# Optimization experiments

Hardware: AMD Instinct MI355X
Metric: run time of the kernel (lower is better)

The kernel has to match this reference:

```python
import jax, jax.numpy as jnp
import numpy as np

B = 32; NPG = 500; N = B * NPG; E = 256000; F = 1024; OD = 128
DD = 80; TD = 32; NH = 4; DH = TD // NH; DFF = 128; NL = 2
LSUB = 128; MAXLEN = 4 * LSUB
NEG = -1e9; SLOPE = 0.01; EPS = 1e-5


def setup_inputs() -> dict:
    key = jax.random.key(0)
    ks = iter(jax.random.split(key, 64))
    nrm = lambda *s: jax.random.normal(next(ks), s, jnp.float32)
    w = lambda *s: nrm(*s) * 0.02
    inp = {}
    inp["pro1_x"] = nrm(N, F)
    inp["pro2_x"] = nrm(N, F)
    inp["pro1_edge_index"] = jax.random.randint(next(ks), (2, E), 0, N)
    inp["pro2_edge_index"] = jax.random.randint(next(ks), (2, E), 0, N)
    inp["pro1_batch"] = jnp.repeat(jnp.arange(B), NPG)
    inp["pro2_batch"] = jnp.repeat(jnp.arange(B), NPG)
    for nm in ("mas1_straight", "mas1_flipped", "mas2_straight", "mas2_flipped"):
        inp[nm] = nrm(B, LSUB, DD)
        inp[nm + "_lengths"] = jax.random.randint(next(ks), (B,), 1, LSUB + 1)
    inp["gcn1_w"] = w(F, F); inp["gcn1_b"] = jnp.zeros(F)
    inp["gcn2_w"] = w(F, F); inp["gcn2_b"] = jnp.zeros(F)
    inp["fc1_w"] = w(OD, F); inp["fc1_b"] = jnp.zeros(OD)
    inp["fc2_w"] = w(OD, F); inp["fc2_b"] = jnp.zeros(OD)
    inp["red_w"] = w(TD - 2, DD); inp["red_b"] = jnp.zeros(TD - 2)
    inp["attn_in_w"] = w(NL, 3 * TD, TD); inp["attn_in_b"] = jnp.zeros((NL, 3 * TD))
    inp["attn_out_w"] = w(NL, TD, TD); inp["attn_out_b"] = jnp.zeros((NL, TD))
    inp["ln1_w"] = jnp.ones((NL, TD)); inp["ln1_b"] = jnp.zeros((NL, TD))
    inp["ln2_w"] = jnp.ones((NL, TD)); inp["ln2_b"] = jnp.zeros((NL, TD))
    inp["ff1_w"] = w(NL, DFF, TD); inp["ff1_b"] = jnp.zeros((NL, DFF))
    inp["ff2_w"] = w(NL, TD, DFF); inp["ff2_b"] = jnp.zeros((NL, TD))
    inp["final_w"] = w(1, 2 * OD + TD); inp["final_b"] = jnp.zeros(1)
    return inp


def _leaky(v):
    return jnp.where(v >= 0, v, SLOPE * v)


def _gcn(x, ei, W, b):
    # GCNConv: x' = D^-1/2 (A + I) D^-1/2 (x @ W^T) + b
    sl = jnp.arange(N, dtype=ei.dtype)
    src = jnp.concatenate([ei[0], sl])
    dst = jnp.concatenate([ei[1], sl])
    deg = jax.ops.segment_sum(jnp.ones(src.shape[0], x.dtype), dst, N)
    dinv = jax.lax.rsqrt(deg)
    norm = (dinv[src] * dinv[dst])[:, None]
    h = x @ W.T
    return jax.ops.segment_sum(h[src] * norm, dst, N) + b


def _gmp(x, batch):
    # global mean pool per graph
    s = jax.ops.segment_sum(x, batch, B)
    c = jax.ops.segment_sum(jnp.ones(x.shape[0], x.dtype), batch, B)
    return s / c[:, None]


def _ln(x, w, b):
    m = x.mean(-1, keepdims=True)
    v = ((x - m) ** 2).mean(-1, keepdims=True)
    return (x - m) * jax.lax.rsqrt(v + EPS) * w + b


def _forward(pro1_x, pro1_edge_index, pro1_batch, pro2_x, pro2_edge_index, pro2_batch,
             mas1_straight, mas1_flipped, mas2_straight, mas2_flipped,
             mas1_straight_lengths, mas1_flipped_lengths, mas2_straight_lengths, mas2_flipped_lengths,
             gcn1_w, gcn1_b, fc1_w, fc1_b, gcn2_w, gcn2_b, fc2_w, fc2_b,
             red_w, red_b, attn_in_w, attn_in_b, attn_out_w, attn_out_b,
             ln1_w, ln1_b, ln2_w, ln2_b, ff1_w, ff1_b, ff2_w, ff2_b,
             final_w, final_b):
    # --- graph branches (dropout = identity at inference) ---
    x1 = _leaky(_gcn(pro1_x, pro1_edge_index, gcn1_w, gcn1_b))
    x1 = _leaky(_gmp(x1, pro1_batch) @ fc1_w.T + fc1_b)           # [B, OD]
    x2 = _leaky(_gcn(pro2_x, pro2_edge_index, gcn2_w, gcn2_b))
    x2 = _leaky(_gmp(x2, pro2_batch) @ fc2_w.T + fc2_b)           # [B, OD]

    # --- vectorized ragged pack: project, append indicators, scatter to offsets ---
    inds = ((1.0, 1.0), (0.0, 1.0), (1.0, 0.0), (0.0, 0.0))      # (straight, first)
    mas = (mas1_straight, mas1_flipped, mas2_straight, mas2_flipped)
    lens = (mas1_straight_lengths, mas1_flipped_lengths, mas2_straight_lengths, mas2_flipped_lengths)
    pos = jnp.arange(LSUB)
    brow = jnp.arange(B)[:, None]
    seq = jnp.zeros((B, MAXLEN, TD), jnp.float32)
    off = jnp.zeros((B,), lens[0].dtype)
    for m, l, (si, fi) in zip(mas, lens, inds):
        proj = m @ red_w.T + red_b                                # [B, LSUB, TD-2]
        ones = jnp.ones((B, LSUB, 1), jnp.float32)
        p = jnp.concatenate([proj, si * ones, fi * ones], -1)    # [B, LSUB, TD]
        valid = pos[None, :] < l[:, None]                        # [B, LSUB]
        idx = jnp.where(valid, off[:, None] + pos[None, :], 0)
        seq = seq.at[brow, idx].add(p * valid[..., None])
        off = off + l
    mask = jnp.arange(MAXLEN)[None, :] < off[:, None]            # [B, MAXLEN] True = valid

    # --- post-norm TransformerEncoder (relu FFN, key padding mask) ---
    x_t = seq
    for li in range(NL):
        qkv = x_t @ attn_in_w[li].T + attn_in_b[li]
        q, k, v = jnp.split(qkv, 3, axis=-1)
        q = q.reshape(B, MAXLEN, NH, DH)
        k = k.reshape(B, MAXLEN, NH, DH)
        v = v.reshape(B, MAXLEN, NH, DH)
        scores = jnp.einsum('bqhd,bkhd->bhqk', q, k) / np.float32(np.sqrt(DH))
        scores = jnp.where(mask[:, None, None, :], scores, NEG)
        attn = jax.nn.softmax(scores, axis=-1)
        o = jnp.einsum('bhqk,bkhd->bqhd', attn, v).reshape(B, MAXLEN, TD)
        o = o @ attn_out_w[li].T + attn_out_b[li]
        x_t = _ln(x_t + o, ln1_w[li], ln1_b[li])
        h = jax.nn.relu(x_t @ ff1_w[li].T + ff1_b[li]) @ ff2_w[li].T + ff2_b[li]
        x_t = _ln(x_t + h, ln2_w[li], ln2_b[li])

    mf = mask[..., None].astype(jnp.float32)
    mas_out = (x_t * mf).sum(1) / mf.sum(1)                      # masked mean [B, TD]

    combined = jnp.concatenate([x1, x2, mas_out], axis=1)        # [B, 2*OD + TD]
    return combined @ final_w.T + final_b                        # [B, 1]


def reference(pro1_x, pro1_edge_index, pro1_batch, pro2_x, pro2_edge_index, pro2_batch,
              mas1_straight, mas1_flipped, mas2_straight, mas2_flipped,
              mas1_straight_lengths, mas1_flipped_lengths, mas2_straight_lengths, mas2_flipped_lengths,
              gcn1_w, gcn1_b, fc1_w, fc1_b, gcn2_w, gcn2_b, fc2_w, fc2_b,
              red_w, red_b, attn_in_w, attn_in_b, attn_out_w, attn_out_b,
              ln1_w, ln1_b, ln2_w, ln2_b, ff1_w, ff1_b, ff2_w, ff2_b,
              final_w, final_b):
    return _forward(pro1_x, pro1_edge_index, pro1_batch, pro2_x, pro2_edge_index, pro2_batch,
                    mas1_straight, mas1_flipped, mas2_straight, mas2_flipped,
                    mas1_straight_lengths, mas1_flipped_lengths, mas2_straight_lengths, mas2_flipped_lengths,
                    gcn1_w, gcn1_b, fc1_w, fc1_b, gcn2_w, gcn2_b, fc2_w, fc2_b,
                    red_w, red_b, attn_in_w, attn_in_b, attn_out_w, attn_out_b,
                    ln1_w, ln1_b, ln2_w, ln2_b, ff1_w, ff1_b, ff2_w, ff2_b,
                    final_w, final_b)
```

## Files before the change

### kernel.cpp

```cpp
#include <hip/hip_runtime.h>
#include <stdint.h>

#define N_NODES 16000
#define MPAD_   16128
#define B_      32
#define NPG_    500
#define E_      256000
#define F_      1024
#define OD_     128
#define DD_     80
#define TD_     32
#define NH_     4
#define DH_     8
#define DFF_    128
#define LSUB_   128
#define MAXLEN_ 512
#define EPS_    1e-5f
#define SLOPE_  0.01f

typedef __bf16 bf16x8 __attribute__((ext_vector_type(8)));
typedef float  f32x4  __attribute__((ext_vector_type(4)));

__device__ __forceinline__ float leaky(float v) { return v >= 0.f ? v : SLOPE_ * v; }

// ... 10 lines not shown

__device__ __forceinline__ void gld_lds16(const void* g, void* l) {
  __builtin_amdgcn_global_load_lds(
      (const __attribute__((address_space(1))) unsigned int*)g,
      (__attribute__((address_space(3))) unsigned int*)l, 16, 0, 0);
}

__global__ void k_prep(const float* __restrict__ x0, const float* __restrict__ x1,
                       const float* __restrict__ w0, const float* __restrict__ w1,
                       unsigned short* __restrict__ xb0, unsigned short* __restrict__ xb1,
                       unsigned short* __restrict__ wb0, unsigned short* __restrict__ wb1,
                       int* __restrict__ cnt, float* __restrict__ pooled) {
  const int y = blockIdx.y;
  int i = blockIdx.x * 256 + threadIdx.x;
  const int stride = gridDim.x * 256;
  if (y == 4) {
    int4 z = make_int4(0, 0, 0, 0);
    for (int idx = i; idx < (2 * N_NODES) / 4; idx += stride) ((int4*)cnt)[idx] = z;
    float4 zf = {0.f, 0.f, 0.f, 0.f};
    for (int idx = i; idx < (2 * B_ * F_) / 4; idx += stride) ((float4*)pooled)[idx] = zf;
    return;
  }
  const float* in = (y == 0) ? x0 : (y == 1) ? x1 : (y == 2) ? w0 : w1;
  unsigned short* out = (y == 0) ? xb0 : (y == 1) ? xb1 : (y == 2) ? wb0 : wb1;
  const int n4 = (y < 2) ? (N_NODES * F_ / 4) : (F_ * F_ / 4);
  for (; i < n4; i += stride) {
    float4 v = ((const float4*)in)[i];
    ushort4 o;
    o.x = f2bf(v.x); o.y = f2bf(v.y); o.z = f2bf(v.z); o.w = f2bf(v.w);
    ((ushort4*)out)[i] = o;
  }
}

#define LDSA(bf, ks, row) (*(const bf16x8*)&lds[(bf)*16384 + (ks)*8192 + (row)*32 + rs])
#define LDSB(bf, ks, row) (*(const bf16x8*)&lds[32768 + (bf)*16384 + (ks)*8192 + (row)*32 + rs])
#define STG_A(bf, R, kti) do { \
  gld_lds16(&Ag[(size_t)(mBase + (R) + r4) * 1024 + (kti) * 64 + c4],      &lds[(bf)*16384 + (R)*32 + t*8]); \
  gld_lds16(&Ag[(size_t)(mBase + (R) + r4) * 1024 + (kti) * 64 + 32 + c4], &lds[(bf)*16384 + 8192 + (R)*32 + t*8]); \
} while (0)
#define STG_B(bf, R, kti) do { \
  gld_lds16(&Bg[(size_t)(nBase + (R) + r4) * 1024 + (kti) * 64 + c4],      &lds[32768 + (bf)*16384 + (R)*32 + t*8]); \
  gld_lds16(&Bg[(size_t)(nBase + (R) + r4) * 1024 + (kti) * 64 + 32 + c4], &lds[32768 + (bf)*16384 + 8192 + (R)*32 + t*8]); \
} while (0)
#define RD_Q0(bf) do { \
  _Pragma("unroll") for (int mi = 0; mi < 4; ++mi) \
  _Pragma("unroll") for (int ks = 0; ks < 2; ++ks) \
    aLo[mi][ks] = LDSA(bf, ks, wrow * 128 + mi * 16 + l15); \
  _Pragma("unroll") for (int ni = 0; ni < 2; ++ni) \
  _Pragma("unroll") for (int ks = 0; ks < 2; ++ks) \
    bLo[ni][ks] = LDSB(bf, ks, wcol * 64 + ni * 16 + l15); \
} while (0)
#define RD_BHI(bf) do { \
  _Pragma("unroll") for (int ni = 0; ni < 2; ++ni) \
  _Pragma("unroll") for (int ks = 0; ks < 2; ++ks) \
    bHi[ni][ks] = LDSB(bf, ks, wcol * 64 + (2 + ni) * 16 + l15); \
} while (0)
#define RD_AHI(bf) do { \
  _Pragma("unroll") for (int mi = 0; mi < 4; ++mi) \
  _Pragma("unroll") for (int ks = 0; ks < 2; ++ks) \
    aHi[mi][ks] = LDSA(bf, ks, wrow * 128 + (4 + mi) * 16 + l15); \
} while (0)
#define MM_Q0() do { __builtin_amdgcn_s_setprio(1); \
  _Pragma("unroll") for (int mi = 0; mi < 4; ++mi) \
  _Pragma("unroll") for (int ni = 0; ni < 2; ++ni) \
  _Pragma("unroll") for (int ks = 0; ks < 2; ++ks) \
    acc[mi][ni] = __builtin_amdgcn_mfma_f32_16x16x32_bf16(aLo[mi][ks], bLo[ni][ks], acc[mi][ni], 0, 0, 0); \
  __builtin_amdgcn_s_setprio(0); } while (0)
#define MM_Q1() do { __builtin_amdgcn_s_setprio(1); \
  _Pragma("unroll") for (int mi = 0; mi < 4; ++mi) \
  _Pragma("unroll") for (int ni = 0; ni < 2; ++ni) \
  _Pragma("unroll") for (int ks = 0; ks < 2; ++ks) \
    acc[mi][2 + ni] = __builtin_amdgcn_mfma_f32_16x16x32_bf16(aLo[mi][ks], bHi[ni][ks], acc[mi][2 + ni], 0, 0, 0); \
  __builtin_amdgcn_s_setprio(0); } while (0)
#define MM_Q3() do { __builtin_amdgcn_s_setprio(1); \
  _Pragma("unroll") for (int mi = 0; mi < 4; ++mi) \
  _Pragma("unroll") for (int ni = 0; ni < 2; ++ni) \
  _Pragma("unroll") for (int ks = 0; ks < 2; ++ks) \
    acc[4 + mi][2 + ni] = __builtin_amdgcn_mfma_f32_16x16x32_bf16(aHi[mi][ks], bHi[ni][ks], acc[4 + mi][2 + ni], 0, 0, 0); \
  __builtin_amdgcn_s_setprio(0); } while (0)
#define MM_Q2() do { __builtin_amdgcn_s_setprio(1); \
  _Pragma("unroll") for (int mi = 0; mi < 4; ++mi) \
  _Pragma("unroll") for (int ni = 0; ni < 2; ++ni) \
  _Pragma("unroll") for (int ks = 0; ks < 2; ++ks) \
    acc[4 + mi][ni] = __builtin_amdgcn_mfma_f32_16x16x32_bf16(aHi[mi][ks], bLo[ni][ks], acc[4 + mi][ni], 0, 0, 0); \
  __builtin_amdgcn_s_setprio(0); } while (0)
#define BAR() do { __builtin_amdgcn_sched_barrier(0); __builtin_amdgcn_s_barrier(); \
                   __builtin_amdgcn_sched_barrier(0); } while (0)
#define LGKM0() do { asm volatile("s_waitcnt lgkmcnt(0)" ::: "memory"); \
                     __builtin_amdgcn_sched_barrier(0); } while (0)
#define VM4() do { asm volatile("s_waitcnt vmcnt(4)" ::: "memory"); } while (0)
#define VM0() do { asm volatile("s_waitcnt vmcnt(0)" ::: "memory"); } while (0)

__global__ __launch_bounds__(512, 2) void k_gemm256(const unsigned short* __restrict__ Ag,
                                                    const unsigned short* __restrict__ Bg,
                                                    unsigned short* __restrict__ Cg) {
  __shared__ short lds[65536];
  const int j  = blockIdx.x;
  const int x8 = j & 7;
  const int chunk = (x8 < 4) ? x8 * 32 : 128 + (x8 - 4) * 31;
  const int pos = chunk + (j >> 3);
  const int mb = pos >> 2, nb = pos & 3;
  const size_t g = blockIdx.z;
  Ag += g * (size_t)MPAD_ * 1024;
  Bg += g * (size_t)1024 * 1024;
  Cg += g * (size_t)MPAD_ * 1024;
  const int t = threadIdx.x;
  const int lane = t & 63, wave = t >> 6;
  const int wrow = wave >> 2, wcol = wave & 3;
  const int quad = lane >> 4, l15 = lane & 15;
  const int mBase = mb * 256, nBase = nb * 256;
  const int r4 = t >> 2;
  const int c4 = (((t & 3) - ((t >> 3) & 3)) & 3) * 8;
  const int rs = ((quad + (l15 >> 1)) & 3) * 8;

  f32x4 acc[8][4];
  f32x4 zero = {0.f, 0.f, 0.f, 0.f};
#pragma unroll
  for (int i = 0; i < 8; ++i)
#pragma unroll
    for (int jn = 0; jn < 4; ++jn) acc[i][jn] = zero;

  bf16x8 aLo[4][2], aHi[4][2], bLo[2][2], bHi[2][2];

  STG_A(0, 0, 0); STG_A(0, 128, 0); STG_B(0, 0, 0); STG_B(0, 128, 0);
  STG_B(1, 0, 1); STG_B(1, 128, 1);
  VM4();
  BAR();

  for (int kt = 0; kt < 16; kt += 2) {
// ... 3 lines not shown
    STG_A(1, 0, kt + 1);
    BAR(); LGKM0(); MM_Q0(); BAR();
    RD_BHI(0);
    STG_A(1, 128, kt + 1);
    BAR(); LGKM0(); MM_Q1(); BAR();
    RD_AHI(0);
    if (s2) STG_B(0, 0, kt + 2);
    BAR(); LGKM0(); MM_Q3(); BAR();
    if (s2) { STG_B(0, 128, kt + 2); VM4(); } else VM0();
    BAR(); MM_Q2(); BAR();
    RD_Q0(1);
    if (s2) STG_A(0, 0, kt + 2);
    BAR(); LGKM0(); MM_Q0(); BAR();
    RD_BHI(1);
    if (s2) STG_A(0, 128, kt + 2);
    BAR(); LGKM0(); MM_Q1(); BAR();
    RD_AHI(1);
    if (s3) STG_B(1, 0, kt + 3);
    BAR(); LGKM0(); MM_Q3(); BAR();
    if (s3) { STG_B(1, 128, kt + 3); VM4(); }
    BAR(); MM_Q2(); BAR();
  }

#pragma unroll
  for (int mi = 0; mi < 8; ++mi)
#pragma unroll
    for (int ni = 0; ni < 4; ++ni)
#pragma unroll
      for (int r = 0; r < 4; ++r) {
        int grow = mBase + wrow * 128 + mi * 16 + quad * 4 + r;
        int gcol = nBase + wcol * 64 + ni * 16 + l15;
        Cg[(size_t)grow * 1024 + gcol] = f2bf(acc[mi][ni][r]);
      }
}

__global__ void k_hist(const int* __restrict__ ei0, const int* __restrict__ ei1,
                       int* __restrict__ cnt, int e, int n) {
  const int g = blockIdx.y;
  const int* dst = (g ? ei1 : ei0) + e;
  int i = blockIdx.x * 256 + threadIdx.x;
  if (i < e) atomicAdd(&cnt[g * n + dst[i]], 1);
}

__global__ void k_scan(const int* __restrict__ cnt_all, int* __restrict__ rowstart_all,
                       int* __restrict__ cursor_all, float* __restrict__ dinv_all, int n) {
  const int g = blockIdx.x;
  const int* cnt = cnt_all + g * n;
  int* rowstart = rowstart_all + g * (n + 1);
  int* cursor   = cursor_all + g * n;
  float* dinv   = dinv_all + g * n;
  __shared__ int part[256];
  __shared__ int base[257];
  int t = threadIdx.x;
  int chunk = (n + 255) >> 8;
  int s = 0;
  for (int j = 0; j < chunk; ++j) {
    int idx = t * chunk + j;
    if (idx < n) s += cnt[idx];
  }
  part[t] = s;
  __syncthreads();
  if (t == 0) {
    int a = 0;
    for (int i = 0; i < 256; ++i) { base[i] = a; a += part[i]; }
    base[256] = a;
  }
  __syncthreads();
  int a = base[t];
  for (int j = 0; j < chunk; ++j) {
    int idx = t * chunk + j;
    if (idx < n) {
      int c = cnt[idx];
      rowstart[idx] = a; cursor[idx] = a; a += c;
      dinv[idx] = rsqrtf((float)c + 1.0f);
    }
  }
  if (t == 0) rowstart[n] = base[256];
}

__global__ void k_scatter(const int* __restrict__ ei0, const int* __restrict__ ei1,
                          const float* __restrict__ dinv_all, int* __restrict__ cursor_all,
                          int2* __restrict__ csre_all, int e, int n) {
  const int g = blockIdx.y;
  const int* ei = g ? ei1 : ei0;
  int i = blockIdx.x * 256 + threadIdx.x;
  if (i < e) {
    int s = ei[i], d = ei[e + i];
    int p = atomicAdd(&cursor_all[g * n + d], 1);
    float w = dinv_all[g * n + s] * dinv_all[g * n + d];
    csre_all[(size_t)g * e + p] = make_int2(s, __float_as_int(w));
  }
}

__global__ __launch_bounds__(256) void k_gather(const uint4* __restrict__ h8_all,
                                                const float* __restrict__ dinv_all,
                                                const int* __restrict__ rowstart_all,
                                                const int2* __restrict__ csre_all,
                                                const float* __restrict__ bias0,
                                                const float* __restrict__ bias1,
                                                float* __restrict__ pooled) {
  const int g = blockIdx.z;
  const uint4* h8 = h8_all + (size_t)g * MPAD_ * 128;
  const float* dinv = dinv_all + (size_t)g * N_NODES;
  const int* rowstart = rowstart_all + (size_t)g * (N_NODES + 1);
  const int2* csre = csre_all + (size_t)g * E_;
  const int sl = blockIdx.x;
  const int t = threadIdx.x;
  const int wv = t >> 6, lane = t & 63;
  const int qtr = lane >> 4, l16 = lane & 15;
  const int i = blockIdx.y * 16 + wv * 4 + qtr;
// ... 36 lines not shown
  pk[0] = leaky(a0 + gbias[f0 + 0]); pk[1] = leaky(a1 + gbias[f0 + 1]);
  pk[2] = leaky(a2 + gbias[f0 + 2]); pk[3] = leaky(a3 + gbias[f0 + 3]);
  pk[4] = leaky(a4 + gbias[f0 + 4]); pk[5] = leaky(a5 + gbias[f0 + 5]);
  pk[6] = leaky(a6 + gbias[f0 + 6]); pk[7] = leaky(a7 + gbias[f0 + 7]);
  __shared__ float sacc[4][16][8];
  const int i0 = blockIdx.y * 16;
  const int b0 = i0 / NPG_, b1 = (i0 + 15) / NPG_;
  const int myb = i / NPG_;
  const int npass = (b0 == b1) ? 1 : 2;
  for (int pass = 0; pass < npass; ++pass) {
    const int bt = pass ? b1 : b0;
    float v[8];
#pragma unroll
    for (int k = 0; k < 8; ++k) {
      float x = (myb == bt) ? pk[k] : 0.f;
      x += __shfl_xor(x, 16);
      x += __shfl_xor(x, 32);
      v[k] = x;
    }
    if (qtr == 0) {
#pragma unroll
      for (int k = 0; k < 8; ++k) sacc[wv][l16][k] = v[k];
    }
    __syncthreads();
    if (t < 128) {
      const int li = t >> 3, kk = t & 7;
      float tot = sacc[0][li][kk] + sacc[1][li][kk] + sacc[2][li][kk] + sacc[3][li][kk];
      atomicAdd(&pooled[(((size_t)g * B_ + bt) << 10) + sl * 128 + t], tot);
    }
    __syncthreads();
  }
}

__global__ __launch_bounds__(256) void k_fc(const float* __restrict__ pooled,
                     const float* __restrict__ w0, const float* __restrict__ w1,
                     const float* __restrict__ bias0, const float* __restrict__ bias1,
                     float* __restrict__ out0, float* __restrict__ out1) {
  __shared__ float ps[F_];
  const int b = blockIdx.x, g = blockIdx.y, t = threadIdx.x;
  const float* p = pooled + ((size_t)g * B_ + b) * F_;
  const float* w = g ? w1 : w0;
  const float* bias = g ? bias1 : bias0;
  float* out = g ? out1 : out0;
  ((float4*)ps)[t] = ((const float4*)p)[t];
  __syncthreads();
  const int wave = t >> 6, lane = t & 63;
  for (int oo = 0; oo < 32; ++oo) {
    const int o = wave * 32 + oo;
    const float* wr = w + (size_t)o * F_;
    float a = 0.f;
#pragma unroll
    for (int c = 0; c < 16; ++c) a += wr[c * 64 + lane] * ps[c * 64 + lane];
#pragma unroll
    for (int m = 1; m < 64; m <<= 1) a += __shfl_xor(a, m, 64);
    if (lane == 0) out[b * OD_ + o] = leaky(a * (1.f / 500.f) + bias[o]);
  }
}

__global__ void k_pack(const float* __restrict__ m0, const float* __restrict__ m1,
                       const float* __restrict__ m2, const float* __restrict__ m3,
                       const int* __restrict__ l0, const int* __restrict__ l1,
                       const int* __restrict__ l2, const int* __restrict__ l3,
                       const float* __restrict__ rw, const float* __restrict__ rb,
                       float* __restrict__ seq, int* __restrict__ tot) {
  __shared__ float xs[DD_];
  const int p = blockIdx.x, b = blockIdx.y, k = blockIdx.z;
  const float* mas = (k == 0) ? m0 : (k == 1) ? m1 : (k == 2) ? m2 : m3;
  const int*   lk  = (k == 0) ? l0 : (k == 1) ? l1 : (k == 2) ? l2 : l3;
  const int len = lk[b];
  if (p >= len) return;
  int off = 0;
  if (k > 0) off += l0[b];
  if (k > 1) off += l1[b];
  if (k > 2) off += l2[b];
  const int t = threadIdx.x;
  if (p == 0 && k == 0 && t == 63) tot[b] = l0[b] + l1[b] + l2[b] + l3[b];
  for (int d = t; d < DD_; d += 64) xs[d] = mas[(size_t)(b * LSUB_ + p) * DD_ + d];
  __syncthreads();
  if (t < TD_) {
    float v;
    if (t < TD_ - 2) {
      float a = rb[t];
      const float* w = &rw[t * DD_];
      for (int d = 0; d < DD_; ++d) a += xs[d] * w[d];
      v = a;
    } else if (t == TD_ - 2) {
      v = (k == 0 || k == 2) ? 1.f : 0.f;
    } else {
      v = (k < 2) ? 1.f : 0.f;
    }
    seq[((size_t)b * MAXLEN_ + off + p) * TD_ + t] = v;
  }
}

__global__ __launch_bounds__(512) void k_qkv(const float* __restrict__ xt,
                                             const float* __restrict__ w,
                                             const float* __restrict__ bias,
                                             const int* __restrict__ tot,
                                             float* __restrict__ Qp,
                                             float* __restrict__ Kp,
                                             float* __restrict__ Vp) {
  __shared__ float xs[4][TD_];
  const int u = threadIdx.x >> 7;
  const int t = threadIdx.x & 127;
  const int row = blockIdx.x * 4 + u;
  const int b = row >> 9, p = row & (MAXLEN_ - 1);
  const bool alive = p < tot[b];
  if (alive && t < TD_) xs[u][t] = xt[(size_t)row * TD_ + t];
  __syncthreads();
  if (!alive || t >= 3 * TD_) return;
  float a = bias[t];
  const float* wr = &w[t * TD_];
#pragma unroll
  for (int k = 0; k < TD_; ++k) a += xs[u][k] * wr[k];
  if (t < 32) {
    Qp[(size_t)row * 32 + t] = a;
  } else if (t < 64) {
    int h = (t - 32) >> 3, d = (t - 32) & 7;
    Kp[(((size_t)b * NH_ + h) * MAXLEN_ + p) * DH_ + d] = a;
  } else {
    int h = (t - 64) >> 3, d = (t - 64) & 7;
    Vp[(((size_t)b * NH_ + h) * MAXLEN_ + p) * DH_ + d] = a;
  }
}

__global__ __launch_bounds__(128) void k_attn(const float* __restrict__ Qp,
                                              const float* __restrict__ Kp,
                                              const float* __restrict__ Vp,
                                              const int* __restrict__ tot,
                                              float* __restrict__ obuf) {
  __shared__ float Kl[MAXLEN_ * DH_];
  __shared__ float Vl[MAXLEN_ * DH_];
  const int h = blockIdx.x, b = blockIdx.y, qz = blockIdx.z;
  const int t = threadIdx.x;
  const int L = tot[b];
  if (qz * 64 >= L) return;
  const float* Kpl = Kp + ((size_t)b * NH_ + h) * MAXLEN_ * DH_;
  const float* Vpl = Vp + ((size_t)b * NH_ + h) * MAXLEN_ * DH_;
  const int n4 = (L * DH_ + 3) >> 2;
  for (int i = t; i < n4; i += 128) {
    ((float4*)Kl)[i] = ((const float4*)Kpl)[i];
    ((float4*)Vl)[i] = ((const float4*)Vpl)[i];
  }
  __syncthreads();
  const int qi = qz * 64 + (t >> 1);
  if (qi >= L) return;
  const int half = t & 1;
  const float scale = 0.35355339059327373f;
  float q[8];
#pragma unroll
  for (int d = 0; d < 8; ++d) q[d] = Qp[((size_t)b * MAXLEN_ + qi) * TD_ + h * 8 + d] * scale;

  float l0 = 0.f, l1 = 0.f;
  float a0[8] = {0, 0, 0, 0, 0, 0, 0, 0};
  float a1[8] = {0, 0, 0, 0, 0, 0, 0, 0};
  int j = half;
  for (; j + 2 < L; j += 4) {
    const float* kr0 = &Kl[j * 8];
    const float* kr1 = &Kl[(j + 2) * 8];
    float s0 = 0.f, s1 = 0.f;
#pragma unroll
    for (int d = 0; d < 8; ++d) { s0 += q[d] * kr0[d]; s1 += q[d] * kr1[d]; }
    float p0 = __expf(s0), p1 = __expf(s1);
    l0 += p0; l1 += p1;
    const float* vr0 = &Vl[j * 8];
    const float* vr1 = &Vl[(j + 2) * 8];
#pragma unroll
    for (int d = 0; d < 8; ++d) { a0[d] += p0 * vr0[d]; a1[d] += p1 * vr1[d]; }
  }
  for (; j < L; j += 2) {
    const float* kr = &Kl[j * 8];
    float s = 0.f;
#pragma unroll
    for (int d = 0; d < 8; ++d) s += q[d] * kr[d];
    float p = __expf(s);
    l0 += p;
    const float* vr = &Vl[j * 8];
#pragma unroll
    for (int d = 0; d < 8; ++d) a0[d] += p * vr[d];
  }
  float l = l0 + l1;
#pragma unroll
  for (int d = 0; d < 8; ++d) a0[d] += a1[d];
  l += __shfl_xor(l, 1);
#pragma unroll
  for (int d = 0; d < 8; ++d) a0[d] += __shfl_xor(a0[d], 1);
  float inv = 1.f / l;
  const int dbase = half * 4;
  float4 o;
  o.x = a0[dbase + 0] * inv; o.y = a0[dbase + 1] * inv;
  o.z = a0[dbase + 2] * inv; o.w = a0[dbase + 3] * inv;
  *(float4*)&obuf[((size_t)b * MAXLEN_ + qi) * TD_ + h * 8 + dbase] = o;
}

__global__ __launch_bounds__(128) void k_post(const float* __restrict__ obuf,
                                              const float* __restrict__ ow,
                                              const float* __restrict__ ob,
                                              const float* __restrict__ l1w,
                                              const float* __restrict__ l1b,
                                              const float* __restrict__ f1w,
                                              const float* __restrict__ f1b,
                                              const float* __restrict__ f2w,
                                              const float* __restrict__ f2b,
                                              const float* __restrict__ l2w,
                                              const float* __restrict__ l2b,
                                              const int* __restrict__ tot,
                                              float* __restrict__ xt) {
  const int t = threadIdx.x;
  const int r0 = blockIdx.x * 4;
  const int b = r0 >> 9;
  const int L = tot[b];
  if ((r0 & (MAXLEN_ - 1)) >= L) return;
  const int u = t >> 5, jj = t & 31;
  const int r = r0 + u;
  const bool alive = (r & (MAXLEN_ - 1)) < L;
  __shared__ float xs[4][TD_];
  __shared__ float hb[4][DFF_];
  if (alive) {
    const float* orow = &obuf[(size_t)r * TD_];
    float a = ob[jj] + xt[(size_t)r * TD_ + jj];
    const float* wr = &ow[jj * TD_];
#pragma unroll
    for (int k = 0; k < TD_; ++k) a += orow[k] * wr[k];
    float s1 = a, s2 = a * a;
#pragma unroll
    for (int m = 1; m < 32; m <<= 1) {
      s1 += __shfl_xor(s1, m, 32);
      s2 += __shfl_xor(s2, m, 32);
    }
    float mean = s1 * (1.f / 32.f);
    float var  = s2 * (1.f / 32.f) - mean * mean;
    xs[u][jj] = (a - mean) * rsqrtf(var + EPS_) * l1w[jj] + l1b[jj];
  }
  __syncthreads();
#pragma unroll
  for (int it = 0; it < 4; ++it) {
    if ((((r0 + it) & (MAXLEN_ - 1)) < L)) {
      float a = f1b[t];
      const float* wr = &f1w[t * TD_];
#pragma unroll
      for (int k = 0; k < TD_; ++k) a += xs[it][k] * wr[k];
      hb[it][t] = fmaxf(a, 0.f);
    }
  }
  __syncthreads();
  if (alive) {
    float a = f2b[jj] + xs[u][jj];
    const float* wr = &f2w[jj * DFF_];
#pragma unroll
    for (int k = 0; k < DFF_; ++k) a += hb[u][k] * wr[k];
    float s1 = a, s2 = a * a;
#pragma unroll
    for (int m = 1; m < 32; m <<= 1) {
      s1 += __shfl_xor(s1, m, 32);
      s2 += __shfl_xor(s2, m, 32);
    }
    float mean = s1 * (1.f / 32.f);
    float var  = s2 * (1.f / 32.f) - mean * mean;
    xt[(size_t)r * TD_ + jj] = (a - mean) * rsqrtf(var + EPS_) * l2w[jj] + l2b[jj];
  }
}

__global__ __launch_bounds__(256) void k_maskfinal(const float* __restrict__ xt,
                                                   const int* __restrict__ tot,
                                                   const float* __restrict__ x1,
                                                   const float* __restrict__ x2,
                                                   const float* __restrict__ fw,
                                                   const float* __restrict__ fb,
                                                   float* __restrict__ out) {
  __shared__ float sbuf[8][32];
  __shared__ float mo[TD_];
  const int b = blockIdx.x, t = threadIdx.x;
  const int j = t & 31, c = t >> 5;
  const int L = tot[b];
  float s = 0.f;
  for (int p = c; p < L; p += 8) s += xt[((size_t)b * MAXLEN_ + p) * TD_ + j];
  sbuf[c][j] = s;
  __syncthreads();
  if (t < 32) {
    float a = 0.f;
#pragma unroll
    for (int cc = 0; cc < 8; ++cc) a += sbuf[cc][t];
    mo[t] = a / (float)L;
  }
  __syncthreads();
  if (t < 64) {
    float s2 = 0.f;
    for (int i = t; i < 2 * OD_ + TD_; i += 64) {
      float cv = (i < OD_) ? x1[b * OD_ + i]
               : (i < 2 * OD_) ? x2[b * OD_ + (i - OD_)]
               : mo[i - 2 * OD_];
      s2 += fw[i] * cv;
    }
#pragma unroll
    for (int m = 1; m < 64; m <<= 1) s2 += __shfl_xor(s2, m, 64);
    if (t == 0) out[b] = s2 + fb[0];
  }
}

extern "C" void kernel_launch(void* const* d_in, const int* in_sizes, int n_in,
                              void* d_out, int out_size, void* d_ws, size_t ws_size,
                              hipStream_t stream) {
  (void)in_sizes; (void)n_in; (void)out_size; (void)ws_size;
  const float* pro_x[2]  = {(const float*)d_in[0], (const float*)d_in[1]};
  const int*   pro_ei[2] = {(const int*)d_in[2], (const int*)d_in[3]};
  const float* mas[4]    = {(const float*)d_in[6], (const float*)d_in[8],
                            (const float*)d_in[10], (const float*)d_in[12]};
  const int*   lens[4]   = {(const int*)d_in[7], (const int*)d_in[9],
                            (const int*)d_in[11], (const int*)d_in[13]};
  const float* gw[2]  = {(const float*)d_in[14], (const float*)d_in[16]};
  const float* gb[2]  = {(const float*)d_in[15], (const float*)d_in[17]};
  const float* fcw[2] = {(const float*)d_in[18], (const float*)d_in[20]};
  const float* fcb[2] = {(const float*)d_in[19], (const float*)d_in[21]};
  const float* red_w = (const float*)d_in[22];
  const float* red_b = (const float*)d_in[23];
  const float* attn_in_w  = (const float*)d_in[24];
  const float* attn_in_b  = (const float*)d_in[25];
  const float* attn_out_w = (const float*)d_in[26];
  const float* attn_out_b = (const float*)d_in[27];
  const float* ln1_w = (const float*)d_in[28];
  const float* ln1_b = (const float*)d_in[29];
  const float* ln2_w = (const float*)d_in[30];
  const float* ln2_b = (const float*)d_in[31];
  const float* ff1_w = (const float*)d_in[32];
  const float* ff1_b = (const float*)d_in[33];
  const float* ff2_w = (const float*)d_in[34];
  const float* ff2_b = (const float*)d_in[35];
  const float* final_w = (const float*)d_in[36];
  const float* final_b = (const float*)d_in[37];
  float* out = (float*)d_out;

  char* p = (char*)d_ws;
  auto carve = [&](size_t bytes) -> void* {
    void* r = (void*)p;
    p += (bytes + 255) & ~(size_t)255;
    return r;
  };
  unsigned short* xb  = (unsigned short*)carve((size_t)2 * MPAD_ * F_ * 2);
  unsigned short* Wb  = (unsigned short*)carve((size_t)2 * F_ * F_ * 2);
  unsigned short* h   = (unsigned short*)carve((size_t)2 * MPAD_ * F_ * 2);
  int*   cnt      = (int*)carve((size_t)2 * N_NODES * 4);
  float* dinv     = (float*)carve((size_t)2 * N_NODES * 4);
  int*   rowstart = (int*)carve((size_t)2 * (N_NODES + 1) * 4);
  int*   cursor   = (int*)carve((size_t)2 * N_NODES * 4);
  int2*  csre     = (int2*)carve((size_t)2 * E_ * 8);
  float* pooled   = (float*)carve((size_t)2 * B_ * F_ * 4);
  float* xg[2];
  xg[0] = (float*)carve((size_t)B_ * OD_ * 4);
  xg[1] = (float*)carve((size_t)B_ * OD_ * 4);
  float* seq    = (float*)carve((size_t)B_ * MAXLEN_ * TD_ * 4);
  float* Qp     = (float*)carve((size_t)B_ * MAXLEN_ * TD_ * 4);
  float* Kp     = (float*)carve((size_t)B_ * NH_ * MAXLEN_ * DH_ * 4);
  float* Vp     = (float*)carve((size_t)B_ * NH_ * MAXLEN_ * DH_ * 4);
  float* obuf   = (float*)carve((size_t)B_ * MAXLEN_ * TD_ * 4);
  int*   totlen = (int*)carve((size_t)B_ * 4);

  k_prep<<<dim3(1024, 5), 256, 0, stream>>>(pro_x[0], pro_x[1], gw[0], gw[1],
                                            xb, xb + (size_t)MPAD_ * F_,
                                            Wb, Wb + (size_t)F_ * F_, cnt, pooled);
  k_gemm256<<<dim3(252, 1, 2), 512, 0, stream>>>(xb, Wb, h);
  k_hist<<<dim3(1000, 2), 256, 0, stream>>>(pro_ei[0], pro_ei[1], cnt, E_, N_NODES);
  k_scan<<<2, 256, 0, stream>>>(cnt, rowstart, cursor, dinv, N_NODES);
  k_scatter<<<dim3(1000, 2), 256, 0, stream>>>(pro_ei[0], pro_ei[1], dinv, cursor,
                                               csre, E_, N_NODES);
  k_gather<<<dim3(8, 1000, 2), 256, 0, stream>>>((const uint4*)h, dinv, rowstart,
                                                 csre, gb[0], gb[1], pooled);
  k_fc<<<dim3(B_, 2), 256, 0, stream>>>(pooled, fcw[0], fcw[1], fcb[0], fcb[1],
                                        xg[0], xg[1]);

  k_pack<<<dim3(LSUB_, B_, 4), 64, 0, stream>>>(mas[0], mas[1], mas[2], mas[3],
                                                lens[0], lens[1], lens[2], lens[3],
                                                red_w, red_b, seq, totlen);

  for (int li = 0; li < 2; ++li) {
    k_qkv<<<(B_ * MAXLEN_) / 4, 512, 0, stream>>>(seq, attn_in_w + (size_t)li * 96 * TD_,
                                                  attn_in_b + (size_t)li * 96, totlen,
                                                  Qp, Kp, Vp);
    k_attn<<<dim3(NH_, B_, 8), 128, 0, stream>>>(Qp, Kp, Vp, totlen, obuf);
    k_post<<<(B_ * MAXLEN_) / 4, 128, 0, stream>>>(
        obuf, attn_out_w + (size_t)li * TD_ * TD_, attn_out_b + (size_t)li * TD_,
        ln1_w + (size_t)li * TD_, ln1_b + (size_t)li * TD_,
        ff1_w + (size_t)li * DFF_ * TD_, ff1_b + (size_t)li * DFF_,
        ff2_w + (size_t)li * TD_ * DFF_, ff2_b + (size_t)li * TD_,
        ln2_w + (size_t)li * TD_, ln2_b + (size_t)li * TD_, totlen, seq);
  }

  k_maskfinal<<<B_, 256, 0, stream>>>(seq, totlen, xg[0], xg[1], final_w, final_b, out);
}
```

Baseline: 734.6 us.

## Fuse transformer branch into one per-graph kernel and fold scan into GEMM

Replaces the pack, per-layer QKV/attention/post kernels, fc and final kernels with a single k_former kernel that runs one 1024-thread block per graph and keeps the sequence in LDS through both layers. K/V are recomputed per head into shared scratch, and the FFN runs in 32-row chunks. The CSR prefix scan is moved into an extra block of the GEMM launch, and the histogram now runs before the GEMM so the scan overlaps GEMM work. This removes about a dozen small launches and their global round trips. In exchange, only 32 blocks run the transformer, so SM utilization is low and each block does serial work over up to 512 rows.

```diff
diff --git a/kernel.cpp b/kernel.cpp
--- a/kernel.cpp
+++ b/kernel.cpp
@@ -66,6 +66,14 @@
   }
 }
 
+__global__ void k_hist(const int* __restrict__ ei0, const int* __restrict__ ei1,
+                       int* __restrict__ cnt, int e, int n) {
+  const int g = blockIdx.y;
+  const int* dst = (g ? ei1 : ei0) + e;
+  int i = blockIdx.x * 256 + threadIdx.x;
+  if (i < e) atomicAdd(&cnt[g * n + dst[i]], 1);
+}
+
 #define LDSA(bf, ks, row) (*(const bf16x8*)&lds[(bf)*16384 + (ks)*8192 + (row)*32 + rs])
 #define LDSB(bf, ks, row) (*(const bf16x8*)&lds[32768 + (bf)*16384 + (ks)*8192 + (row)*32 + rs])
 #define STG_A(bf, R, kti) do { \
@@ -127,8 +135,47 @@
 
 __global__ __launch_bounds__(512, 2) void k_gemm256(const unsigned short* __restrict__ Ag,
                                                     const unsigned short* __restrict__ Bg,
-                                                    unsigned short* __restrict__ Cg) {
+                                                    unsigned short* __restrict__ Cg,
+                                                    const int* __restrict__ cnt_all,
+                                                    int* __restrict__ rowstart_all,
+                                                    int* __restrict__ cursor_all,
+                                                    float* __restrict__ dinv_all) {
   __shared__ short lds[65536];
+  if (blockIdx.x == 252) {
+    const int g2 = blockIdx.z;
+    const int* cnt = cnt_all + g2 * N_NODES;
+    int* rowstart = rowstart_all + g2 * (N_NODES + 1);
+    int* cursor   = cursor_all + g2 * N_NODES;
+    float* dinvp  = dinv_all + g2 * N_NODES;
+    int* ipart = (int*)lds;
+    int* ibase = ipart + 512;
+    const int tt = threadIdx.x;
+    const int CH = 32;
+    int s = 0;
+    for (int j2 = 0; j2 < CH; ++j2) {
+      int idx = tt * CH + j2;
+      if (idx < N_NODES) s += cnt[idx];
+    }
+    ipart[tt] = s;
+    __syncthreads();
+    if (tt == 0) {
+      int a = 0;
+      for (int i2 = 0; i2 < 512; ++i2) { ibase[i2] = a; a += ipart[i2]; }
+      ibase[512] = a;
+    }
+    __syncthreads();
+    int a = ibase[tt];
+    for (int j2 = 0; j2 < CH; ++j2) {
+      int idx = tt * CH + j2;
+      if (idx < N_NODES) {
+        int c = cnt[idx];
+        rowstart[idx] = a; cursor[idx] = a; a += c;
+        dinvp[idx] = rsqrtf((float)c + 1.0f);
+      }
+    }
+    if (tt == 0) rowstart[N_NODES] = ibase[512];
+    return;
+  }
   const int j  = blockIdx.x;
   const int x8 = j & 7;
   const int chunk = (x8 < 4) ? x8 * 32 : 128 + (x8 - 4) * 31;
@@ -198,50 +245,6 @@
         int gcol = nBase + wcol * 64 + ni * 16 + l15;
         Cg[(size_t)grow * 1024 + gcol] = f2bf(acc[mi][ni][r]);
       }
-}
-
-__global__ void k_hist(const int* __restrict__ ei0, const int* __restrict__ ei1,
-                       int* __restrict__ cnt, int e, int n) {
-  const int g = blockIdx.y;
-  const int* dst = (g ? ei1 : ei0) + e;
-  int i = blockIdx.x * 256 + threadIdx.x;
-  if (i < e) atomicAdd(&cnt[g * n + dst[i]], 1);
-}
-
-__global__ void k_scan(const int* __restrict__ cnt_all, int* __restrict__ rowstart_all,
-                       int* __restrict__ cursor_all, float* __restrict__ dinv_all, int n) {
-  const int g = blockIdx.x;
-  const int* cnt = cnt_all + g * n;
-  int* rowstart = rowstart_all + g * (n + 1);
-  int* cursor   = cursor_all + g * n;
-  float* dinv   = dinv_all + g * n;
-  __shared__ int part[256];
-  __shared__ int base[257];
-  int t = threadIdx.x;
-  int chunk = (n + 255) >> 8;
-  int s = 0;
-  for (int j = 0; j < chunk; ++j) {
-    int idx = t * chunk + j;
-    if (idx < n) s += cnt[idx];
-  }
-  part[t] = s;
-  __syncthreads();
-  if (t == 0) {
-    int a = 0;
-    for (int i = 0; i < 256; ++i) { base[i] = a; a += part[i]; }
-    base[256] = a;
-  }
-  __syncthreads();
-  int a = base[t];
-  for (int j = 0; j < chunk; ++j) {
-    int idx = t * chunk + j;
-    if (idx < n) {
-      int c = cnt[idx];
-      rowstart[idx] = a; cursor[idx] = a; a += c;
-      dinv[idx] = rsqrtf((float)c + 1.0f);
-    }
-  }
-  if (t == 0) rowstart[n] = base[256];
 }
 
 __global__ void k_scatter(const int* __restrict__ ei0, const int* __restrict__ ei1,
@@ -344,264 +347,233 @@
   }
 }
 
-__global__ __launch_bounds__(256) void k_fc(const float* __restrict__ pooled,
-                     const float* __restrict__ w0, const float* __restrict__ w1,
-                     const float* __restrict__ bias0, const float* __restrict__ bias1,
-                     float* __restrict__ out0, float* __restrict__ out1) {
-  __shared__ float ps[F_];
-  const int b = blockIdx.x, g = blockIdx.y, t = threadIdx.x;
-  const float* p = pooled + ((size_t)g * B_ + b) * F_;
-  const float* w = g ? w1 : w0;
-  const float* bias = g ? bias1 : bias0;
-  float* out = g ? out1 : out0;
-  ((float4*)ps)[t] = ((const float4*)p)[t];
+__global__ __launch_bounds__(1024, 1) void k_former(
+    const float* __restrict__ m0, const float* __restrict__ m1,
+    const float* __restrict__ m2, const float* __restrict__ m3,
+    const int* __restrict__ l0, const int* __restrict__ l1,
+    const int* __restrict__ l2, const int* __restrict__ l3,
+    const float* __restrict__ rw, const float* __restrict__ rb,
+    const float* __restrict__ attn_in_w, const float* __restrict__ attn_in_b,
+    const float* __restrict__ attn_out_w, const float* __restrict__ attn_out_b,
+    const float* __restrict__ ln1_w, const float* __restrict__ ln1_b,
+    const float* __restrict__ ln2_w, const float* __restrict__ ln2_b,
+    const float* __restrict__ ff1_w, const float* __restrict__ ff1_b,
+    const float* __restrict__ ff2_w, const float* __restrict__ ff2_b,
+    const float* __restrict__ pooled,
+    const float* __restrict__ fcw0, const float* __restrict__ fcw1,
+    const float* __restrict__ fcb0, const float* __restrict__ fcb1,
+    const float* __restrict__ fw, const float* __restrict__ fb,
+    float* __restrict__ out) {
+  __shared__ float xt[512 * 33];
+  __shared__ float scr[8192];
+  const int b = blockIdx.x;
+  const int t = threadIdx.x;
+  const int L0 = l0[b], L1 = l1[b], L2c = l2[b], L3 = l3[b];
+  const int o1 = L0, o2 = L0 + L1, o3 = o2 + L2c, L = o3 + L3;
+
+  {
+    const int gi = t >> 5, ll = t & 31;
+    for (int r = gi; r < L; r += 32) {
+      int k, p;
+      if (r < o1)      { k = 0; p = r; }
+      else if (r < o2) { k = 1; p = r - o1; }
+      else if (r < o3) { k = 2; p = r - o2; }
+      else             { k = 3; p = r - o3; }
+      const float* mas = (k == 0) ? m0 : (k == 1) ? m1 : (k == 2) ? m2 : m3;
+      const float* mrow = mas + ((size_t)b * LSUB_ + p) * DD_;
+      float v;
+      if (ll < TD_ - 2) {
+        float a = rb[ll];
+        const float* w = rw + ll * DD_;
+        for (int d = 0; d < DD_; ++d) a += mrow[d] * w[d];
+        v = a;
+      } else if (ll == TD_ - 2) {
+        v = (k == 0 || k == 2) ? 1.f : 0.f;
+      } else {
+        v = (k < 2) ? 1.f : 0.f;
+      }
+      xt[r * 33 + ll] = v;
+    }
+  }
   __syncthreads();
-  const int wave = t >> 6, lane = t & 63;
-  for (int oo = 0; oo < 32; ++oo) {
-    const int o = wave * 32 + oo;
-    const float* wr = w + (size_t)o * F_;
+
+  const int q = t >> 1, half = t & 1;
+  const float scale = 0.35355339059327373f;
+
+  for (int li = 0; li < 2; ++li) {
+    const float* wi = attn_in_w + (size_t)li * 96 * TD_;
+    const float* bi = attn_in_b + (size_t)li * 96;
+    float oacc[16];
+#pragma unroll
+    for (int h = 0; h < NH_; ++h) {
+      __syncthreads();
+      for (int idx = t; idx < L * DH_; idx += 1024) {
+        int p = idx >> 3, d = idx & 7;
+        const float* wk = wi + (32 + h * 8 + d) * TD_;
+        const float* wv = wi + (64 + h * 8 + d) * TD_;
+        float ak = bi[32 + h * 8 + d], av = bi[64 + h * 8 + d];
+        const float* xr = &xt[p * 33];
+#pragma unroll
+        for (int k = 0; k < TD_; ++k) { float x = xr[k]; ak += x * wk[k]; av += x * wv[k]; }
+        scr[idx] = ak;
+        scr[4096 + idx] = av;
+      }
+      __syncthreads();
+      float lsum = 0.f;
+      float a[8] = {0, 0, 0, 0, 0, 0, 0, 0};
+      if (q < L) {
+        float qv[8];
+        const float* xr = &xt[q * 33];
+#pragma unroll
+        for (int d = 0; d < 8; ++d) {
+          const float* wq = wi + (h * 8 + d) * TD_;
+          float aq = bi[h * 8 + d];
+#pragma unroll
+          for (int k = 0; k < TD_; ++k) aq += xr[k] * wq[k];
+          qv[d] = aq * scale;
+        }
+        for (int jj = half; jj < L; jj += 2) {
+          const float* kr = &scr[jj * 8];
+          float s = 0.f;
+#pragma unroll
+          for (int d = 0; d < 8; ++d) s += qv[d] * kr[d];
+          float pr = __expf(s);
+          lsum += pr;
+          const float* vr = &scr[4096 + jj * 8];
+#pragma unroll
+          for (int d = 0; d < 8; ++d) a[d] += pr * vr[d];
+        }
+      }
+      lsum += __shfl_xor(lsum, 1);
+#pragma unroll
+      for (int d = 0; d < 8; ++d) a[d] += __shfl_xor(a[d], 1);
+      float inv = (q < L) ? 1.f / lsum : 0.f;
+#pragma unroll
+      for (int d = 0; d < 4; ++d) oacc[h * 4 + d] = a[half * 4 + d] * inv;
+    }
+    const float* ow = attn_out_w + (size_t)li * TD_ * TD_;
+    const float* ob = attn_out_b + (size_t)li * TD_;
+    const float* w1 = ff1_w + (size_t)li * DFF_ * TD_;
+    const float* b1 = ff1_b + (size_t)li * DFF_;
+    const float* w2 = ff2_w + (size_t)li * TD_ * DFF_;
+    const float* b2 = ff2_b + (size_t)li * TD_;
+    const float* A1 = ln1_w + (size_t)li * TD_;
+    const float* B1 = ln1_b + (size_t)li * TD_;
+    const float* A2 = ln2_w + (size_t)li * TD_;
+    const float* B2 = ln2_b + (size_t)li * TD_;
+    float* obufc = scr;
+    float* xsc   = scr + 32 * 33;
+    float* hbc   = scr + 64 * 33;
+    for (int c0 = 0; c0 < 512; c0 += 32) {
+      if (c0 >= L) break;
+      __syncthreads();
+      if (q >= c0 && q < c0 + 32 && q < L) {
+        int u = q - c0;
+#pragma unroll
+        for (int h2 = 0; h2 < 4; ++h2)
+#pragma unroll
+          for (int d = 0; d < 4; ++d)
+            obufc[u * 33 + h2 * 8 + half * 4 + d] = oacc[h2 * 4 + d];
+      }
+      __syncthreads();
+      {
+        const int u = t >> 5, jj = t & 31;
+        const int r = c0 + u;
+        const bool alive = r < L;
+        float a_ = 0.f;
+        if (alive) {
+          a_ = ob[jj] + xt[r * 33 + jj];
+          const float* wr = ow + jj * TD_;
+#pragma unroll
+          for (int k = 0; k < TD_; ++k) a_ += obufc[u * 33 + k] * wr[k];
+        }
+        float s1 = a_, s2 = a_ * a_;
+#pragma unroll
+        for (int m = 1; m < 32; m <<= 1) {
+          s1 += __shfl_xor(s1, m, 32);
+          s2 += __shfl_xor(s2, m, 32);
+        }
+        if (alive) {
+          float mean = s1 * (1.f / 32.f);
+          float var  = s2 * (1.f / 32.f) - mean * mean;
+          xsc[u * 33 + jj] = (a_ - mean) * rsqrtf(var + EPS_) * A1[jj] + B1[jj];
+        }
+      }
+      __syncthreads();
+      for (int idx = t; idx < 32 * DFF_; idx += 1024) {
+        const int u = idx >> 7, jj = idx & 127;
+        if (c0 + u < L) {
+          float a_ = b1[jj];
+          const float* wr = w1 + jj * TD_;
+#pragma unroll
+          for (int k = 0; k < TD_; ++k) a_ += xsc[u * 33 + k] * wr[k];
+          hbc[u * 128 + jj] = fmaxf(a_, 0.f);
+        }
+      }
+      __syncthreads();
+      {
+        const int u = t >> 5, jj = t & 31;
+        const int r = c0 + u;
+        const bool alive = r < L;
+        float a_ = 0.f;
+        if (alive) {
+          a_ = b2[jj] + xsc[u * 33 + jj];
+          const float* wr = w2 + jj * DFF_;
+#pragma unroll
+          for (int k = 0; k < DFF_; ++k) a_ += hbc[u * 128 + k] * wr[k];
+        }
+        float s1 = a_, s2 = a_ * a_;
+#pragma unroll
+        for (int m = 1; m < 32; m <<= 1) {
+          s1 += __shfl_xor(s1, m, 32);
+          s2 += __shfl_xor(s2, m, 32);
+        }
+        if (alive) {
+          float mean = s1 * (1.f / 32.f);
+          float var  = s2 * (1.f / 32.f) - mean * mean;
+          xt[r * 33 + jj] = (a_ - mean) * rsqrtf(var + EPS_) * A2[jj] + B2[jj];
+        }
+      }
+    }
+    __syncthreads();
+  }
+
+  float* xf = scr + 1200;
+  {
+    const int g2 = t >> 9, rest = t & 511;
+    const int o = rest >> 2, sub = t & 3;
+    const float* pp = pooled + ((size_t)g2 * B_ + b) * F_;
+    const float* wrow = (g2 ? fcw1 : fcw0) + (size_t)o * F_;
     float a = 0.f;
-#pragma unroll
-    for (int c = 0; c < 16; ++c) a += wr[c * 64 + lane] * ps[c * 64 + lane];
-#pragma unroll
-    for (int m = 1; m < 64; m <<= 1) a += __shfl_xor(a, m, 64);
-    if (lane == 0) out[b * OD_ + o] = leaky(a * (1.f / 500.f) + bias[o]);
-  }
-}
-
-__global__ void k_pack(const float* __restrict__ m0, const float* __restrict__ m1,
-                       const float* __restrict__ m2, const float* __restrict__ m3,
-                       const int* __restrict__ l0, const int* __restrict__ l1,
-                       const int* __restrict__ l2, const int* __restrict__ l3,
-                       const float* __restrict__ rw, const float* __restrict__ rb,
-                       float* __restrict__ seq, int* __restrict__ tot) {
-  __shared__ float xs[DD_];
-  const int p = blockIdx.x, b = blockIdx.y, k = blockIdx.z;
-  const float* mas = (k == 0) ? m0 : (k == 1) ? m1 : (k == 2) ? m2 : m3;
-  const int*   lk  = (k == 0) ? l0 : (k == 1) ? l1 : (k == 2) ? l2 : l3;
-  const int len = lk[b];
-  if (p >= len) return;
-  int off = 0;
-  if (k > 0) off += l0[b];
-  if (k > 1) off += l1[b];
-  if (k > 2) off += l2[b];
-  const int t = threadIdx.x;
-  if (p == 0 && k == 0 && t == 63) tot[b] = l0[b] + l1[b] + l2[b] + l3[b];
-  for (int d = t; d < DD_; d += 64) xs[d] = mas[(size_t)(b * LSUB_ + p) * DD_ + d];
-  __syncthreads();
-  if (t < TD_) {
-    float v;
-    if (t < TD_ - 2) {
-      float a = rb[t];
-      const float* w = &rw[t * DD_];
-      for (int d = 0; d < DD_; ++d) a += xs[d] * w[d];
-      v = a;
-    } else if (t == TD_ - 2) {
-      v = (k == 0 || k == 2) ? 1.f : 0.f;
-    } else {
-      v = (k < 2) ? 1.f : 0.f;
-    }
-    seq[((size_t)b * MAXLEN_ + off + p) * TD_ + t] = v;
-  }
-}
-
-__global__ __launch_bounds__(512) void k_qkv(const float* __restrict__ xt,
-                                             const float* __restrict__ w,
-                                             const float* __restrict__ bias,
-                                             const int* __restrict__ tot,
-                                             float* __restrict__ Qp,
-                                             float* __restrict__ Kp,
-                                             float* __restrict__ Vp) {
-  __shared__ float xs[4][TD_];
-  const int u = threadIdx.x >> 7;
-  const int t = threadIdx.x & 127;
-  const int row = blockIdx.x * 4 + u;
-  const int b = row >> 9, p = row & (MAXLEN_ - 1);
-  const bool alive = p < tot[b];
-  if (alive && t < TD_) xs[u][t] = xt[(size_t)row * TD_ + t];
-  __syncthreads();
-  if (!alive || t >= 3 * TD_) return;
-  float a = bias[t];
-  const float* wr = &w[t * TD_];
-#pragma unroll
-  for (int k = 0; k < TD_; ++k) a += xs[u][k] * wr[k];
-  if (t < 32) {
-    Qp[(size_t)row * 32 + t] = a;
-  } else if (t < 64) {
-    int h = (t - 32) >> 3, d = (t - 32) & 7;
-    Kp[(((size_t)b * NH_ + h) * MAXLEN_ + p) * DH_ + d] = a;
-  } else {
-    int h = (t - 64) >> 3, d = (t - 64) & 7;
-    Vp[(((size_t)b * NH_ + h) * MAXLEN_ + p) * DH_ + d] = a;
-  }
-}
-
-__global__ __launch_bounds__(128) void k_attn(const float* __restrict__ Qp,
-                                              const float* __restrict__ Kp,
-                                              const float* __restrict__ Vp,
-                                              const int* __restrict__ tot,
-                                              float* __restrict__ obuf) {
-  __shared__ float Kl[MAXLEN_ * DH_];
-  __shared__ float Vl[MAXLEN_ * DH_];
-  const int h = blockIdx.x, b = blockIdx.y, qz = blockIdx.z;
-  const int t = threadIdx.x;
-  const int L = tot[b];
-  if (qz * 64 >= L) return;
-  const float* Kpl = Kp + ((size_t)b * NH_ + h) * MAXLEN_ * DH_;
-  const float* Vpl = Vp + ((size_t)b * NH_ + h) * MAXLEN_ * DH_;
-  const int n4 = (L * DH_ + 3) >> 2;
-  for (int i = t; i < n4; i += 128) {
-    ((float4*)Kl)[i] = ((const float4*)Kpl)[i];
-    ((float4*)Vl)[i] = ((const float4*)Vpl)[i];
-  }
-  __syncthreads();
-  const int qi = qz * 64 + (t >> 1);
-  if (qi >= L) return;
-  const int half = t & 1;
-  const float scale = 0.35355339059327373f;
-  float q[8];
-#pragma unroll
-  for (int d = 0; d < 8; ++d) q[d] = Qp[((size_t)b * MAXLEN_ + qi) * TD_ + h * 8 + d] * scale;
-
-  float l0 = 0.f, l1 = 0.f;
-  float a0[8] = {0, 0, 0, 0, 0, 0, 0, 0};
-  float a1[8] = {0, 0, 0, 0, 0, 0, 0, 0};
-  int j = half;
-  for (; j + 2 < L; j += 4) {
-    const float* kr0 = &Kl[j * 8];
-    const float* kr1 = &Kl[(j + 2) * 8];
-    float s0 = 0.f, s1 = 0.f;
-#pragma unroll
-    for (int d = 0; d < 8; ++d) { s0 += q[d] * kr0[d]; s1 += q[d] * kr1[d]; }
-    float p0 = __expf(s0), p1 = __expf(s1);
-    l0 += p0; l1 += p1;
-    const float* vr0 = &Vl[j * 8];
-    const float* vr1 = &Vl[(j + 2) * 8];
-#pragma unroll
-    for (int d = 0; d < 8; ++d) { a0[d] += p0 * vr0[d]; a1[d] += p1 * vr1[d]; }
-  }
-  for (; j < L; j += 2) {
-    const float* kr = &Kl[j * 8];
+    for (int kk = 0; kk < 256; ++kk) {
+      int k = sub * 256 + kk;
+      a += pp[k] * wrow[k];
+    }
+    a += __shfl_xor(a, 1, 4);
+    a += __shfl_xor(a, 2, 4);
+    if (sub == 0)
+      xf[g2 * 128 + o] = leaky(a * (1.f / 500.f) + (g2 ? fcb1 : fcb0)[o]);
+  }
+  float* sb = scr;
+  float* mo = scr + 1056;
+  {
+    const int c = t >> 5, jj = t & 31;
     float s = 0.f;
-#pragma unroll
-    for (int d = 0; d < 8; ++d) s += q[d] * kr[d];
-    float p = __expf(s);
-    l0 += p;
-    const float* vr = &Vl[j * 8];
-#pragma unroll
-    for (int d = 0; d < 8; ++d) a0[d] += p * vr[d];
-  }
-  float l = l0 + l1;
-#pragma unroll
-  for (int d = 0; d < 8; ++d) a0[d] += a1[d];
-  l += __shfl_xor(l, 1);
-#pragma unroll
-  for (int d = 0; d < 8; ++d) a0[d] += __shfl_xor(a0[d], 1);
-  float inv = 1.f / l;
-  const int dbase = half * 4;
-  float4 o;
-  o.x = a0[dbase + 0] * inv; o.y = a0[dbase + 1] * inv;
-  o.z = a0[dbase + 2] * inv; o.w = a0[dbase + 3] * inv;
-  *(float4*)&obuf[((size_t)b * MAXLEN_ + qi) * TD_ + h * 8 + dbase] = o;
-}
-
-__global__ __launch_bounds__(128) void k_post(const float* __restrict__ obuf,
-                                              const float* __restrict__ ow,
-                                              const float* __restrict__ ob,
-                                              const float* __restrict__ l1w,
-                                              const float* __restrict__ l1b,
-                                              const float* __restrict__ f1w,
-                                              const float* __restrict__ f1b,
-                                              const float* __restrict__ f2w,
-                                              const float* __restrict__ f2b,
-                                              const float* __restrict__ l2w,
-                                              const float* __restrict__ l2b,
-                                              const int* __restrict__ tot,
-                                              float* __restrict__ xt) {
-  const int t = threadIdx.x;
-  const int r0 = blockIdx.x * 4;
-  const int b = r0 >> 9;
-  const int L = tot[b];
-  if ((r0 & (MAXLEN_ - 1)) >= L) return;
-  const int u = t >> 5, jj = t & 31;
-  const int r = r0 + u;
-  const bool alive = (r & (MAXLEN_ - 1)) < L;
-  __shared__ float xs[4][TD_];
-  __shared__ float hb[4][DFF_];
-  if (alive) {
-    const float* orow = &obuf[(size_t)r * TD_];
-    float a = ob[jj] + xt[(size_t)r * TD_ + jj];
-    const float* wr = &ow[jj * TD_];
-#pragma unroll
-    for (int k = 0; k < TD_; ++k) a += orow[k] * wr[k];
-    float s1 = a, s2 = a * a;
-#pragma unroll
-    for (int m = 1; m < 32; m <<= 1) {
-      s1 += __shfl_xor(s1, m, 32);
-      s2 += __shfl_xor(s2, m, 32);
-    }
-    float mean = s1 * (1.f / 32.f);
-    float var  = s2 * (1.f / 32.f) - mean * mean;
-    xs[u][jj] = (a - mean) * rsqrtf(var + EPS_) * l1w[jj] + l1b[jj];
-  }
-  __syncthreads();
-#pragma unroll
-  for (int it = 0; it < 4; ++it) {
-    if ((((r0 + it) & (MAXLEN_ - 1)) < L)) {
-      float a = f1b[t];
-      const float* wr = &f1w[t * TD_];
-#pragma unroll
-      for (int k = 0; k < TD_; ++k) a += xs[it][k] * wr[k];
-      hb[it][t] = fmaxf(a, 0.f);
-    }
-  }
-  __syncthreads();
-  if (alive) {
-    float a = f2b[jj] + xs[u][jj];
-    const float* wr = &f2w[jj * DFF_];
-#pragma unroll
-    for (int k = 0; k < DFF_; ++k) a += hb[u][k] * wr[k];
-    float s1 = a, s2 = a * a;
-#pragma unroll
-    for (int m = 1; m < 32; m <<= 1) {
-      s1 += __shfl_xor(s1, m, 32);
-      s2 += __shfl_xor(s2, m, 32);
-    }
-    float mean = s1 * (1.f / 32.f);
-    float var  = s2 * (1.f / 32.f) - mean * mean;
-    xt[(size_t)r * TD_ + jj] = (a - mean) * rsqrtf(var + EPS_) * l2w[jj] + l2b[jj];
-  }
-}
-
-__global__ __launch_bounds__(256) void k_maskfinal(const float* __restrict__ xt,
-                                                   const int* __restrict__ tot,
-                                                   const float* __restrict__ x1,
-                                                   const float* __restrict__ x2,
-                                                   const float* __restrict__ fw,
-                                                   const float* __restrict__ fb,
-                                                   float* __restrict__ out) {
-  __shared__ float sbuf[8][32];
-  __shared__ float mo[TD_];
-  const int b = blockIdx.x, t = threadIdx.x;
-  const int j = t & 31, c = t >> 5;
-  const int L = tot[b];
-  float s = 0.f;
-  for (int p = c; p < L; p += 8) s += xt[((size_t)b * MAXLEN_ + p) * TD_ + j];
-  sbuf[c][j] = s;
+    for (int r = c; r < L; r += 32) s += xt[r * 33 + jj];
+    sb[c * 33 + jj] = s;
+  }
   __syncthreads();
   if (t < 32) {
     float a = 0.f;
 #pragma unroll
-    for (int cc = 0; cc < 8; ++cc) a += sbuf[cc][t];
+    for (int c = 0; c < 32; ++c) a += sb[c * 33 + t];
     mo[t] = a / (float)L;
   }
   __syncthreads();
   if (t < 64) {
     float s2 = 0.f;
     for (int i = t; i < 2 * OD_ + TD_; i += 64) {
-      float cv = (i < OD_) ? x1[b * OD_ + i]
-               : (i < 2 * OD_) ? x2[b * OD_ + (i - OD_)]
-               : mo[i - 2 * OD_];
+      float cv = (i < 256) ? xf[i] : mo[i - 256];
       s2 += fw[i] * cv;
     }
 #pragma unroll
@@ -657,45 +629,22 @@
   int*   cursor   = (int*)carve((size_t)2 * N_NODES * 4);
   int2*  csre     = (int2*)carve((size_t)2 * E_ * 8);
   float* pooled   = (float*)carve((size_t)2 * B_ * F_ * 4);
-  float* xg[2];
-  xg[0] = (float*)carve((size_t)B_ * OD_ * 4);
-  xg[1] = (float*)carve((size_t)B_ * OD_ * 4);
-  float* seq    = (float*)carve((size_t)B_ * MAXLEN_ * TD_ * 4);
-  float* Qp     = (float*)carve((size_t)B_ * MAXLEN_ * TD_ * 4);
-  float* Kp     = (float*)carve((size_t)B_ * NH_ * MAXLEN_ * DH_ * 4);
-  float* Vp     = (float*)carve((size_t)B_ * NH_ * MAXLEN_ * DH_ * 4);
-  float* obuf   = (float*)carve((size_t)B_ * MAXLEN_ * TD_ * 4);
-  int*   totlen = (int*)carve((size_t)B_ * 4);
 
   k_prep<<<dim3(1024, 5), 256, 0, stream>>>(pro_x[0], pro_x[1], gw[0], gw[1],
                                             xb, xb + (size_t)MPAD_ * F_,
                                             Wb, Wb + (size_t)F_ * F_, cnt, pooled);
-  k_gemm256<<<dim3(252, 1, 2), 512, 0, stream>>>(xb, Wb, h);
   k_hist<<<dim3(1000, 2), 256, 0, stream>>>(pro_ei[0], pro_ei[1], cnt, E_, N_NODES);
-  k_scan<<<2, 256, 0, stream>>>(cnt, rowstart, cursor, dinv, N_NODES);
+  k_gemm256<<<dim3(253, 1, 2), 512, 0, stream>>>(xb, Wb, h, cnt, rowstart, cursor, dinv);
   k_scatter<<<dim3(1000, 2), 256, 0, stream>>>(pro_ei[0], pro_ei[1], dinv, cursor,
                                                csre, E_, N_NODES);
   k_gather<<<dim3(8, 1000, 2), 256, 0, stream>>>((const uint4*)h, dinv, rowstart,
                                                  csre, gb[0], gb[1], pooled);
-  k_fc<<<dim3(B_, 2), 256, 0, stream>>>(pooled, fcw[0], fcw[1], fcb[0], fcb[1],
-                                        xg[0], xg[1]);
-
-  k_pack<<<dim3(LSUB_, B_, 4), 64, 0, stream>>>(mas[0], mas[1], mas[2], mas[3],
-                                                lens[0], lens[1], lens[2], lens[3],
-                                                red_w, red_b, seq, totlen);
-
-  for (int li = 0; li < 2; ++li) {
-    k_qkv<<<(B_ * MAXLEN_) / 4, 512, 0, stream>>>(seq, attn_in_w + (size_t)li * 96 * TD_,
-                                                  attn_in_b + (size_t)li * 96, totlen,
-                                                  Qp, Kp, Vp);
-    k_attn<<<dim3(NH_, B_, 8), 128, 0, stream>>>(Qp, Kp, Vp, totlen, obuf);
-    k_post<<<(B_ * MAXLEN_) / 4, 128, 0, stream>>>(
-        obuf, attn_out_w + (size_t)li * TD_ * TD_, attn_out_b + (size_t)li * TD_,
-        ln1_w + (size_t)li * TD_, ln1_b + (size_t)li * TD_,
-        ff1_w + (size_t)li * DFF_ * TD_, ff1_b + (size_t)li * DFF_,
-        ff2_w + (size_t)li * TD_ * DFF_, ff2_b + (size_t)li * TD_,
-        ln2_w + (size_t)li * TD_, ln2_b + (size_t)li * TD_, totlen, seq);
-  }
-
-  k_maskfinal<<<B_, 256, 0, stream>>>(seq, totlen, xg[0], xg[1], final_w, final_b, out);
-}
+  k_former<<<B_, 1024, 0, stream>>>(mas[0], mas[1], mas[2], mas[3],
+                                    lens[0], lens[1], lens[2], lens[3],
+                                    red_w, red_b,
+                                    attn_in_w, attn_in_b, attn_out_w, attn_out_b,
+                                    ln1_w, ln1_b, ln2_w, ln2_b,
+                                    ff1_w, ff1_b, ff2_w, ff2_b,
+                                    pooled, fcw[0], fcw[1], fcb[0], fcb[1],
+                                    final_w, final_b, out);
+}
```

Result: slower. 1.968 ms (+167.9%).
